# Kernel tuning notes

Measured on AMD Instinct MI355X. Metric: run time of the kernel, lower is better.

## Reference

```python
import jax, jax.numpy as jnp
import numpy as np

N_NODES = 10000
N_EDGES = 80000
IN_DIM = 768
HID = 256
HEADS = 8
NEG_SLOPE = 0.2


def setup_inputs() -> dict:
    key = jax.random.key(0)
    ks = jax.random.split(key, 12)
    s = 0.02
    x = jax.random.normal(ks[0], (N_NODES, IN_DIM), dtype=jnp.float32)
    edge_index = jax.random.randint(ks[1], (2, N_EDGES), 0, N_NODES, dtype=jnp.int64)
    W1 = jax.random.normal(ks[2], (IN_DIM, HEADS * HID), dtype=jnp.float32) * s
    a_src1 = jax.random.normal(ks[3], (HEADS, HID), dtype=jnp.float32) * s
    a_dst1 = jax.random.normal(ks[4], (HEADS, HID), dtype=jnp.float32) * s
    b1 = jnp.zeros((HEADS * HID,), dtype=jnp.float32)
    W2 = jax.random.normal(ks[5], (HEADS * HID, HEADS * HID), dtype=jnp.float32) * s
    a_src2 = jax.random.normal(ks[6], (HEADS, HID), dtype=jnp.float32) * s
    a_dst2 = jax.random.normal(ks[7], (HEADS, HID), dtype=jnp.float32) * s
    b2 = jnp.zeros((HID,), dtype=jnp.float32)
    # graph_projection: 256 -> 256
    Wp = jax.random.normal(ks[8], (HID, HID), dtype=jnp.float32) * s
    bp = jnp.zeros((HID,), dtype=jnp.float32)
    return dict(x=x, edge_index=edge_index, W1=W1, a_src1=a_src1, a_dst1=a_dst1,
                b1=b1, W2=W2, a_src2=a_src2, a_dst2=a_dst2, b2=b2, Wp=Wp, bp=bp)


def _gat_conv(x, src, dst, W, a_src, a_dst, b, concat):
    """PyG GATConv (eval mode, self-loops already appended to src/dst)."""
    N = x.shape[0]
    H, C = a_src.shape
    h = (x @ W).reshape(N, H, C)                         # [N,H,C] per-head projection
    alpha_s = jnp.sum(h * a_src[None], axis=-1)           # [N,H]
    alpha_d = jnp.sum(h * a_dst[None], axis=-1)           # [N,H]
    e = jax.nn.leaky_relu(alpha_s[src] + alpha_d[dst], NEG_SLOPE)  # [E,H]
    # segment softmax over incoming edges of each dst node
    m = jax.ops.segment_max(e, dst, num_segments=N)       # [N,H]
    m = jnp.where(jnp.isfinite(m), m, 0.0)
    p = jnp.exp(e - m[dst])
    denom = jax.ops.segment_sum(p, dst, num_segments=N)   # [N,H]
    alpha = p / (denom[dst] + 1e-16)                      # [E,H]
    out = jax.ops.segment_sum(alpha[:, :, None] * h[src], dst, num_segments=N)  # [N,H,C]
    if concat:
        return out.reshape(N, H * C) + b
    return out.mean(axis=1) + b


def reference(x, edge_index, W1, a_src1, a_dst1, b1, W2, a_src2, a_dst2, b2, Wp, bp):
    N = x.shape[0]
    loops = jnp.arange(N, dtype=edge_index.dtype)
    src = jnp.concatenate([edge_index[0], loops])
    dst = jnp.concatenate([edge_index[1], loops])
    h = _gat_conv(x, src, dst, W1, a_src1, a_dst1, b1, concat=True)   # [N, 2048]
    h = jax.nn.elu(h)                                                 # dropout: eval/no-op
    h = _gat_conv(h, src, dst, W2, a_src2, a_dst2, b2, concat=False)  # [N, 256]
    h = h @ Wp + bp
    return jax.nn.relu(h)                                             # dropout: eval/no-op
```

## Files before the change

### kernel.cpp

```cpp
#include <hip/hip_runtime.h>
#include <cstdint>
#include <cstddef>

#define IN_DIM  768
#define NNODES  10000
#define MPAD    10240
#define NEDGES  80000
#define E_TOT   90000
#define HEADS   8
#define HID     256
#define HC      2048
#define NEG_SLOPE 0.2f

#define CVT_BLK  ((MPAD * IN_DIM / 4) / 256)
#define CNT_BLK  ((E_TOT + 255) / 256)
#define T1_BLK   ((HC / 32) * (IN_DIM / 32))
#define T2_BLK   ((HC / 32) * (HC / 32))
#define TP_BLK   ((HID / 32) * (HID / 32))
#define PREP_BLK (CVT_BLK + CNT_BLK + T1_BLK + T2_BLK + TP_BLK)

typedef _Float16 __attribute__((ext_vector_type(8))) f16x8;
typedef float    __attribute__((ext_vector_type(4))) f32x4;

__device__ __forceinline__ int edge_src(const int* __restrict__ ei, int e) {
    return (e < NEDGES) ? ei[e] : (e - NEDGES);
}
__device__ __forceinline__ int edge_dst(const int* __restrict__ ei, int e) {
    return (e < NEDGES) ? ei[NEDGES + e] : (e - NEDGES);
}

__device__ __forceinline__ void tcvt_body(
    const float* __restrict__ W, _Float16* __restrict__ T,
    int K, int N, int bx, int by, int t)
{
    __shared__ float tile[32][33];
    int tx = t & 31, ty = t >> 5;
#pragma unroll
    for (int q = 0; q < 4; q++)
        tile[ty + q * 8][tx] = W[(size_t)(by * 32 + ty + q * 8) * N + bx * 32 + tx];
    __syncthreads();
#pragma unroll
    for (int q = 0; q < 4; q++) {
        float v = tile[tx][ty + q * 8];
        T[(size_t)(bx * 32 + ty + q * 8) * K + by * 32 + tx] = (_Float16)v;
    }
}

__global__ __launch_bounds__(256) void prep_kernel(
    const float* __restrict__ x, _Float16* __restrict__ xh,
    const int* __restrict__ ei, int* __restrict__ cnt,
    const float* __restrict__ W1, _Float16* __restrict__ W1t,
    const float* __restrict__ W2, _Float16* __restrict__ W2t,
    const float* __restrict__ Wp, _Float16* __restrict__ Wpt)
{
    int b = blockIdx.x;
    int t = threadIdx.x;
    if (b < CVT_BLK) {
        int i = b * 256 + t;
        size_t e = (size_t)i * 4;
        int r = (int)(e / IN_DIM);
        float4 v = (r < NNODES) ? *(const float4*)(x + e)
                                : make_float4(0.f, 0.f, 0.f, 0.f);
        _Float16 h4[4] = {(_Float16)v.x, (_Float16)v.y, (_Float16)v.z, (_Float16)v.w};
        *(ushort4*)(xh + e) = *(ushort4*)h4;
    } else if (b < CVT_BLK + CNT_BLK) {
        int e = (b - CVT_BLK) * 256 + t;
        if (e < E_TOT) atomicAdd(&cnt[edge_dst(ei, e)], 1);
    } else if (b < CVT_BLK + CNT_BLK + T1_BLK) {
        int idx = b - (CVT_BLK + CNT_BLK);
        tcvt_body(W1, W1t, IN_DIM, HC, idx % (HC / 32), idx / (HC / 32), t);
    } else if (b < CVT_BLK + CNT_BLK + T1_BLK + T2_BLK) {
        int idx = b - (CVT_BLK + CNT_BLK + T1_BLK);
        tcvt_body(W2, W2t, HC, HC, idx % (HC / 32), idx / (HC / 32), t);
    } else {
        int idx = b - (CVT_BLK + CNT_BLK + T1_BLK + T2_BLK);
        tcvt_body(Wp, Wpt, HID, HID, idx % (HID / 32), idx / (HID / 32), t);
    }
}

__global__ void scan_kernel(const int* __restrict__ cnt, int* __restrict__ indptr) {
    __shared__ int sums[1024];
    const int CH = 10;
    int t = threadIdx.x;
    int base = t * CH;
    int s = 0;
#pragma unroll
    for (int i = 0; i < CH; i++) { int idx = base + i; if (idx < NNODES) s += cnt[idx]; }
    sums[t] = s;
    __syncthreads();
    for (int off = 1; off < 1024; off <<= 1) {
        int v = (t >= off) ? sums[t - off] : 0;
        __syncthreads();
        sums[t] += v;
        __syncthreads();
    }
    int run = (t == 0) ? 0 : sums[t - 1];
#pragma unroll
    for (int i = 0; i < CH; i++) {
        int idx = base + i;
        if (idx < NNODES) { indptr[idx] = run; run += cnt[idx]; }
    }
    if (t == 0) indptr[NNODES] = E_TOT;
}

__global__ void scatter_kernel(const int* __restrict__ ei, const int* __restrict__ indptr,
                               int* __restrict__ cur, int* __restrict__ sorted) {
    int e = blockIdx.x * 256 + threadIdx.x;
    if (e < E_TOT) {
        int d = edge_dst(ei, e);
        int pos = atomicAdd(&cur[d], 1);
        sorted[indptr[d] + pos] = e;
    }
}

__global__ __launch_bounds__(512, 2) void gemm8p_kernel(
    const _Float16* __restrict__ A, const _Float16* __restrict__ B,
    _Float16* __restrict__ C, int M, int K, int Nn)
{
    __shared__ __align__(16) _Float16 lds[2][36864];

    const int t = threadIdx.x;
    const int w = t >> 6, lane = t & 63;
    const int fr = lane & 15, q4 = lane >> 4;
    const int wr = w >> 2, wc = w & 3;

    const int nwgx = gridDim.x;
    int wg = blockIdx.y * nwgx + blockIdx.x;
    const int cpx = (nwgx * gridDim.y) >> 3;
    wg = (wg & 7) * cpx + (wg >> 3);
    const int row0 = (wg / nwgx) * 320;
    const int col0 = (wg % nwgx) * 256;

    const int rowt = t >> 3;
    const int scol = ((t & 7) ^ (rowt & 7)) << 3;
    const _Float16* baseA = A + (size_t)(row0 + rowt) * K + scol;
    const _Float16* baseB = B + (size_t)(col0 + rowt) * K + scol;
    const int dstw = w * 512;

    auto stageA = [&](int q, int kel, int bb) {
        __builtin_amdgcn_global_load_lds(
            (const __attribute__((address_space(1))) void*)(baseA + (size_t)q * 64 * K + kel),
            (__attribute__((address_space(3))) void*)&lds[bb][q * 4096 + dstw], 16, 0, 0);
    };
    auto stageB = [&](int q, int kel, int bb) {
        __builtin_amdgcn_global_load_lds(
            (const __attribute__((address_space(1))) void*)(baseB + (size_t)q * 64 * K + kel),
            (__attribute__((address_space(3))) void*)&lds[bb][20480 + q * 4096 + dstw], 16, 0, 0);
    };

    f32x4 acc[2][2][5][2];
#pragma unroll
    for (int qm = 0; qm < 2; qm++)
#pragma unroll
        for (int qn = 0; qn < 2; qn++)
#pragma unroll
            for (int mi = 0; mi < 5; mi++)
#pragma unroll
                for (int ni = 0; ni < 2; ni++)
                    acc[qm][qn][mi][ni] = {0.f, 0.f, 0.f, 0.f};

    f16x8 fa[5][2], fb[2][2];

#define LOADA(BB, QM)                                                           \
    {                                                                           \
        _Pragma("unroll")                                                       \
        for (int mi = 0; mi < 5; mi++) {                                        \
            _Pragma("unroll")                                                   \
            for (int ks = 0; ks < 2; ks++) {                                    \
                int lr = wr * 80 + mi * 16 + fr;                                \
                int sl = ((ks << 2) | q4) ^ (fr & 7);                           \
                fa[mi][ks] = *(const f16x8*)&lds[BB][(QM) * 10240 + (lr << 6) + (sl << 3)]; \
            }                                                                   \
        }                                                                       \
    }
#define LOADB(BB, QN)                                                           \
    {                                                                           \
        _Pragma("unroll")                                                       \
        for (int ni = 0; ni < 2; ni++) {                                        \
            _Pragma("unroll")                                                   \
            for (int ks = 0; ks < 2; ks++) {                                    \
                int lr = wc * 32 + ni * 16 + fr;                                \
                int sl = ((ks << 2) | q4) ^ (fr & 7);                           \
                fb[ni][ks] = *(const f16x8*)&lds[BB][20480 + (QN) * 8192 + (lr << 6) + (sl << 3)]; \
            }                                                                   \
        }                                                                       \
    }

#define PHASE(QM, QN, LOAD_STMT, STAGE_STMT, WAIT_STMT)                         \
    do {                                                                        \
        WAIT_STMT;                                                              \
        __builtin_amdgcn_s_barrier();                                           \
        LOAD_STMT;                                                              \
        STAGE_STMT;                                                             \
        asm volatile("s_waitcnt lgkmcnt(0)" ::: "memory");                      \
        __builtin_amdgcn_sched_barrier(0);                                      \
        __builtin_amdgcn_s_setprio(1);                                          \
        _Pragma("unroll")                                                       \
        for (int ks = 0; ks < 2; ks++) {                                        \
            _Pragma("unroll")                                                   \
            for (int mi = 0; mi < 5; mi++) {                                    \
                _Pragma("unroll")                                               \
                for (int ni = 0; ni < 2; ni++)                                  \
                    acc[QM][QN][mi][ni] = __builtin_amdgcn_mfma_f32_16x16x32_f16(\
                        fa[mi][ks], fb[ni][ks], acc[QM][QN][mi][ni], 0, 0, 0);  \
            }                                                                   \
        }                                                                       \
        __builtin_amdgcn_s_setprio(0);                                          \
        __builtin_amdgcn_sched_barrier(0);                                      \
    } while (0)

#define VM(N) asm volatile("s_waitcnt vmcnt(" #N ")" ::: "memory")

    stageA(0, 0, 0); stageA(1, 0, 0); stageA(2, 0, 0);
    stageB(0, 0, 0); stageB(1, 0, 0);
    stageB(2, 0, 0); stageB(3, 0, 0);
    stageA(3, 0, 0); stageA(4, 0, 0);

    const int nT = K >> 6;
    int t0 = 0;
    for (; t0 < nT - 1; ++t0) {
        int bb = t0 & 1;
        int bn = bb ^ 1;
        int k1 = (t0 + 1) << 6;
        PHASE(0, 0, { LOADA(bb, 0); LOADB(bb, 0); },
              { stageA(0, k1, bn); stageA(1, k1, bn); stageA(2, k1, bn); },
              VM(4));
        PHASE(0, 1, { LOADB(bb, 1); },
              { stageB(0, k1, bn); stageB(1, k1, bn); },
              VM(5));
        PHASE(1, 1, { LOADA(bb, 1); },
              { stageB(2, k1, bn); stageB(3, k1, bn); },
              VM(5));
        PHASE(1, 0, { LOADB(bb, 0); },
              { stageA(3, k1, bn); stageA(4, k1, bn); },
              ((void)0));
    }
    {
        int bb = t0 & 1;
        PHASE(0, 0, { LOADA(bb, 0); LOADB(bb, 0); }, ((void)0), VM(4));
        PHASE(0, 1, { LOADB(bb, 1); },               ((void)0), VM(2));
        PHASE(1, 1, { LOADA(bb, 1); },               ((void)0), VM(0));
        PHASE(1, 0, { LOADB(bb, 0); },               ((void)0), ((void)0));
    }
#undef PHASE
#undef LOADA
#undef LOADB
#undef VM

#pragma unroll
    for (int qm = 0; qm < 2; qm++)
#pragma unroll
        for (int qn = 0; qn < 2; qn++)
#pragma unroll
            for (int mi = 0; mi < 5; mi++) {
                int mb = row0 + qm * 160 + wr * 80 + mi * 16 + q4 * 4;
#pragma unroll
                for (int ni = 0; ni < 2; ni++) {
                    int n = col0 + qn * 128 + wc * 32 + ni * 16 + fr;
#pragma unroll
                    for (int r = 0; r < 4; r++) {
                        int m = mb + r;
                        if (m < M) C[(size_t)m * Nn + n] = (_Float16)acc[qm][qn][mi][ni][r];
                    }
                }
            }
}

template <int EPI>
__global__ __launch_bounds__(256) void mfma_gemm_kernel(
    const _Float16* __restrict__ A, const _Float16* __restrict__ B,
    void* __restrict__ Cout, const float* __restrict__ bias,
    int M, int K, int Nn, int swz)
{
    __shared__ __align__(16) _Float16 sA[2][128 * 32];
    __shared__ __align__(16) _Float16 sB[2][128 * 32];

    int t = threadIdx.x;
    int bx = blockIdx.x, by = blockIdx.y;
    if (swz) {
        int id = by * 16 + bx;
        int xcd = id & 7, slot = id >> 3;
        bx = 2 * xcd + (slot & 1);
        by = slot >> 1;
    }
    int row0 = by * 128;
    int col0 = bx * 128;

    int s0 = t, s1 = t + 256;
    int m0 = s0 >> 2, k0 = (s0 & 3) * 8;
    int m1 = s1 >> 2, k1 = (s1 & 3) * 8;
    const _Float16* a0 = A + (size_t)(row0 + m0) * K + k0;
    const _Float16* a1 = A + (size_t)(row0 + m1) * K + k1;
    const _Float16* b0 = B + (size_t)(col0 + m0) * K + k0;
    const _Float16* b1 = B + (size_t)(col0 + m1) * K + k1;

    int w = t >> 6, lane = t & 63;
    int wm = (w & 1) * 64, wn = (w >> 1) * 64;
    int fr = lane & 15, quad = lane >> 4;

    auto stage = [&](int kt, int bsel) {
        _Float16* dA0 = &sA[bsel][(w * 64) * 8];
        _Float16* dA1 = &sA[bsel][(w * 64 + 256) * 8];
        _Float16* dB0 = &sB[bsel][(w * 64) * 8];
        _Float16* dB1 = &sB[bsel][(w * 64 + 256) * 8];
        __builtin_amdgcn_global_load_lds(
            (const __attribute__((address_space(1))) void*)(a0 + kt),
            (__attribute__((address_space(3))) void*)dA0, 16, 0, 0);
        __builtin_amdgcn_global_load_lds(
            (const __attribute__((address_space(1))) void*)(a1 + kt),
            (__attribute__((address_space(3))) void*)dA1, 16, 0, 0);
        __builtin_amdgcn_global_load_lds(
            (const __attribute__((address_space(1))) void*)(b0 + kt),
            (__attribute__((address_space(3))) void*)dB0, 16, 0, 0);
        __builtin_amdgcn_global_load_lds(
            (const __attribute__((address_space(1))) void*)(b1 + kt),
            (__attribute__((address_space(3))) void*)dB1, 16, 0, 0);
    };

    f32x4 acc[4][4];
#pragma unroll
    for (int i = 0; i < 4; i++)
#pragma unroll
        for (int j = 0; j < 4; j++) acc[i][j] = {0.f, 0.f, 0.f, 0.f};

    const int nIt = K / 32;
    stage(0, 0);
    __syncthreads();

    for (int it = 0; it < nIt; ++it) {
        int cb = it & 1;
        if (it + 1 < nIt) stage((it + 1) * 32, cb ^ 1);

        f16x8 fa[4], fb[4];
#pragma unroll
        for (int i = 0; i < 4; i++) {
            fa[i] = *(const f16x8*)&sA[cb][(wm + i * 16 + fr) * 32 + quad * 8];
            fb[i] = *(const f16x8*)&sB[cb][(wn + i * 16 + fr) * 32 + quad * 8];
        }
#pragma unroll
        for (int i = 0; i < 4; i++)
#pragma unroll
            for (int j = 0; j < 4; j++)
                acc[i][j] = __builtin_amdgcn_mfma_f32_16x16x32_f16(fa[i], fb[j], acc[i][j], 0, 0, 0);

        if (it + 1 < nIt) __syncthreads();
    }

    if (EPI == 0) {
        _Float16* C = (_Float16*)Cout;
#pragma unroll
        for (int i = 0; i < 4; i++) {
            int mbase = row0 + wm + i * 16 + quad * 4;
#pragma unroll
            for (int j = 0; j < 4; j++) {
                int n = col0 + wn + j * 16 + fr;
#pragma unroll
                for (int r = 0; r < 4; r++) {
                    int m = mbase + r;
                    if (m < M) C[(size_t)m * Nn + n] = (_Float16)acc[i][j][r];
                }
            }
        }
    } else {
        float* C = (float*)Cout;
        float bv[4];
#pragma unroll
        for (int j = 0; j < 4; j++) bv[j] = bias[col0 + wn + j * 16 + fr];
#pragma unroll
        for (int i = 0; i < 4; i++) {
            int mbase = row0 + wm + i * 16 + quad * 4;
#pragma unroll
            for (int j = 0; j < 4; j++) {
                int n = col0 + wn + j * 16 + fr;
#pragma unroll
                for (int r = 0; r < 4; r++) {
                    int m = mbase + r;
                    if (m < M) C[(size_t)m * Nn + n] = fmaxf(acc[i][j][r] + bv[j], 0.f);
                }
            }
        }
    }
}

__global__ __launch_bounds__(256) void attn_kernel(
    const _Float16* __restrict__ H, const float* __restrict__ a_src,
    const float* __restrict__ a_dst, float* __restrict__ as_out,
    float* __restrict__ ad_out)
{
    int n = blockIdx.x;
    int t = threadIdx.x;
    int h = t >> 5, l = t & 31;
    f16x8 hv = *(const f16x8*)&H[(size_t)n * HC + h * HID + l * 8];
    const float* asp = a_src + h * HID + l * 8;
    const float* adp = a_dst + h * HID + l * 8;
    float sa = 0.f, sd = 0.f;
#pragma unroll
    for (int q = 0; q < 8; q++) {
        float v = (float)hv[q];
        sa = fmaf(v, asp[q], sa);
        sd = fmaf(v, adp[q], sd);
    }
#pragma unroll
    for (int o = 16; o > 0; o >>= 1) {
        sa += __shfl_xor(sa, o, 32);
        sd += __shfl_xor(sd, o, 32);
    }
    if (l == 0) { as_out[n * HEADS + h] = sa; ad_out[n * HEADS + h] = sd; }
}

template <int MODE>
__global__ __launch_bounds__(256) void agg_kernel(
    const _Float16* __restrict__ H, const float* __restrict__ as_,
    const float* __restrict__ ad_, const float* __restrict__ bias,
    const int* __restrict__ indptr, const int* __restrict__ sorted,
    const int* __restrict__ ei, _Float16* __restrict__ outh)
{
    __shared__ float m8[HEADS], d8[HEADS], adl[HEADS];
    __shared__ int   srcl[64];
    __shared__ float al2[HEADS][64];
    __shared__ float red[HC];

    int n = blockIdx.x;
    int t = threadIdx.x;

    if (n >= NNODES) {
        if (MODE == 0) {
            _Float16 z8[8] = {};
            *(f16x8*)&outh[(size_t)n * HC + t * 8] = *(f16x8*)z8;
        } else {
            outh[(size_t)n * HID + t] = (_Float16)0.f;
        }
        return;
    }

    int start = indptr[n];
    int deg = indptr[n + 1] - start;

    if (t < HEADS) adl[t] = ad_[n * HEADS + t];
    __syncthreads();

    int hh = t >> 5, c8 = (t & 31) * 8;
    const size_t hoff = (size_t)hh * HID + c8;
    float acc[8] = {};

    if (deg <= 64) {
        if (t < deg) srcl[t] = edge_src(ei, sorted[start + t]);
        __syncthreads();
        {
            int j = t & 63, h0 = t >> 6;
            if (j < deg) {
                int s = srcl[j];
#pragma unroll
                for (int q = 0; q < 2; q++) {
                    int hx = h0 + q * 4;
                    float v = as_[s * HEADS + hx] + adl[hx];
                    v = (v >= 0.f) ? v : NEG_SLOPE * v;
                    al2[hx][j] = v;
                }
            }
        }
        __syncthreads();
        {
            int h = t >> 5, l = t & 31;
            float mx = -1e30f;
            for (int jj = l; jj < deg; jj += 32) mx = fmaxf(mx, al2[h][jj]);
#pragma unroll
            for (int o = 16; o > 0; o >>= 1) mx = fmaxf(mx, __shfl_xor(mx, o, 32));
            float sm = 0.f;
            for (int jj = l; jj < deg; jj += 32) {
                float e = expf(al2[h][jj] - mx);
                al2[h][jj] = e;
                sm += e;
            }
#pragma unroll
            for (int o = 16; o > 0; o >>= 1) sm += __shfl_xor(sm, o, 32);
            float den = sm + 1e-16f;
            for (int jj = l; jj < deg; jj += 32) al2[h][jj] = al2[h][jj] / den;
        }
        __syncthreads();
        int jj = 0;
        for (; jj + 3 < deg; jj += 4) {
            int sx0 = srcl[jj + 0], sx1 = srcl[jj + 1];
            int sx2 = srcl[jj + 2], sx3 = srcl[jj + 3];
            f16x8 h0v = *(const f16x8*)&H[(size_t)sx0 * HC + hoff];
            f16x8 h1v = *(const f16x8*)&H[(size_t)sx1 * HC + hoff];
            f16x8 h2v = *(const f16x8*)&H[(size_t)sx2 * HC + hoff];
            f16x8 h3v = *(const f16x8*)&H[(size_t)sx3 * HC + hoff];
            float4 a4 = *(const float4*)&al2[hh][jj];
#pragma unroll
            for (int q = 0; q < 8; q++) acc[q] = fmaf(a4.x, (float)h0v[q], acc[q]);
#pragma unroll
            for (int q = 0; q < 8; q++) acc[q] = fmaf(a4.y, (float)h1v[q], acc[q]);
#pragma unroll
            for (int q = 0; q < 8; q++) acc[q] = fmaf(a4.z, (float)h2v[q], acc[q]);
#pragma unroll
            for (int q = 0; q < 8; q++) acc[q] = fmaf(a4.w, (float)h3v[q], acc[q]);
        }
        for (; jj < deg; jj++) {
            int s = srcl[jj];
            f16x8 hv = *(const f16x8*)&H[(size_t)s * HC + hoff];
            float a = al2[hh][jj];
#pragma unroll
            for (int q = 0; q < 8; q++)
                acc[q] = fmaf(a, (float)hv[q], acc[q]);
        }
    } else {
        int h = t >> 5, l = t & 31;
        float adh = adl[h];

        float mx = -1e30f;
        for (int j = l; j < deg; j += 32) {
            int e = sorted[start + j];
            int s = edge_src(ei, e);
            float v = as_[s * HEADS + h] + adh;
            v = (v >= 0.f) ? v : NEG_SLOPE * v;
            mx = fmaxf(mx, v);
        }
#pragma unroll
        for (int o = 16; o > 0; o >>= 1) mx = fmaxf(mx, __shfl_xor(mx, o, 32));

        float sm = 0.f;
        for (int j = l; j < deg; j += 32) {
            int e = sorted[start + j];
            int s = edge_src(ei, e);
            float v = as_[s * HEADS + h] + adh;
            v = (v >= 0.f) ? v : NEG_SLOPE * v;
            sm += expf(v - mx);
        }
#pragma unroll
        for (int o = 16; o > 0; o >>= 1) sm += __shfl_xor(sm, o, 32);
        if (l == 0) { m8[h] = mx; d8[h] = sm; }

        for (int base = 0; base < deg; base += 64) {
            int cntc = min(64, deg - base);
            __syncthreads();
            if (t < cntc) srcl[t] = edge_src(ei, sorted[start + base + t]);
            __syncthreads();
            {
                int j = t & 63, h0 = t >> 6;
                if (j < cntc) {
                    int s = srcl[j];
#pragma unroll
                    for (int q = 0; q < 2; q++) {
                        int hx = h0 + q * 4;
                        float v = as_[s * HEADS + hx] + adl[hx];
                        v = (v >= 0.f) ? v : NEG_SLOPE * v;
                        al2[hx][j] = expf(v - m8[hx]) / (d8[hx] + 1e-16f);
                    }
                }
            }
            __syncthreads();
            int jj = 0;
            for (; jj + 3 < cntc; jj += 4) {
                int sx0 = srcl[jj + 0], sx1 = srcl[jj + 1];
                int sx2 = srcl[jj + 2], sx3 = srcl[jj + 3];
                f16x8 h0v = *(const f16x8*)&H[(size_t)sx0 * HC + hoff];
                f16x8 h1v = *(const f16x8*)&H[(size_t)sx1 * HC + hoff];
                f16x8 h2v = *(const f16x8*)&H[(size_t)sx2 * HC + hoff];
                f16x8 h3v = *(const f16x8*)&H[(size_t)sx3 * HC + hoff];
                float4 a4 = *(const float4*)&al2[hh][jj];
#pragma unroll
                for (int q = 0; q < 8; q++) acc[q] = fmaf(a4.x, (float)h0v[q], acc[q]);
#pragma unroll
                for (int q = 0; q < 8; q++) acc[q] = fmaf(a4.y, (float)h1v[q], acc[q]);
#pragma unroll
                for (int q = 0; q < 8; q++) acc[q] = fmaf(a4.z, (float)h2v[q], acc[q]);
#pragma unroll
                for (int q = 0; q < 8; q++) acc[q] = fmaf(a4.w, (float)h3v[q], acc[q]);
            }
            for (; jj < cntc; jj++) {
                int s = srcl[jj];
                f16x8 hv = *(const f16x8*)&H[(size_t)s * HC + hoff];
                float a = al2[hh][jj];
#pragma unroll
                for (int q = 0; q < 8; q++)
                    acc[q] = fmaf(a, (float)hv[q], acc[q]);
            }
        }
    }

    if (MODE == 0) {
        _Float16 o8[8];
#pragma unroll
        for (int q = 0; q < 8; q++) {
            float v = acc[q] + bias[hoff + q];
            v = (v > 0.f) ? v : expm1f(v);
            o8[q] = (_Float16)v;
        }
        *(f16x8*)&outh[(size_t)n * HC + hoff] = *(f16x8*)o8;
    } else {
#pragma unroll
        for (int q = 0; q < 8; q++) red[hoff + q] = acc[q];
        __syncthreads();
        float s = 0.f;
#pragma unroll
        for (int h2 = 0; h2 < HEADS; h2++) s += red[h2 * HID + t];
        outh[(size_t)n * HID + t] = (_Float16)(s * 0.125f + bias[t]);
    }
}

extern "C" void kernel_launch(void* const* d_in, const int* in_sizes, int n_in,
                              void* d_out, int out_size, void* d_ws, size_t ws_size,
                              hipStream_t stream)
{
    const float* x      = (const float*)d_in[0];
    const int*   ei     = (const int*)  d_in[1];
    const float* W1     = (const float*)d_in[2];
    const float* a_src1 = (const float*)d_in[3];
    const float* a_dst1 = (const float*)d_in[4];
    const float* b1     = (const float*)d_in[5];
    const float* W2     = (const float*)d_in[6];
    const float* a_src2 = (const float*)d_in[7];
    const float* a_dst2 = (const float*)d_in[8];
    const float* b2     = (const float*)d_in[9];
    const float* Wp     = (const float*)d_in[10];
    const float* bp     = (const float*)d_in[11];
    float* out = (float*)d_out;

    char* ws = (char*)d_ws;
    size_t off = 0;
    auto alloc = [&](size_t bytes) -> char* {
        char* p = ws + off;
        off += (bytes + 255) & ~(size_t)255;
        return p;
    };
    _Float16* Hbuf = (_Float16*)alloc((size_t)NNODES * HC * 2);
    _Float16* A2   = (_Float16*)alloc((size_t)MPAD * HC * 2);
    _Float16* W1t  = (_Float16*)alloc((size_t)HC * IN_DIM * 2);
    _Float16* W2t  = (_Float16*)alloc((size_t)HC * HC * 2);
    _Float16* Wpt  = (_Float16*)alloc((size_t)HID * HID * 2);
    _Float16* xh   = (_Float16*)alloc((size_t)MPAD * IN_DIM * 2);
    _Float16* out2h = (_Float16*)alloc((size_t)MPAD * HID * 2);
    float* asad   = (float*)alloc((size_t)4 * NNODES * HEADS * sizeof(float));
    float* as1 = asad;
    float* ad1 = asad + (size_t)NNODES * HEADS;
    float* as2 = asad + (size_t)2 * NNODES * HEADS;
    float* ad2 = asad + (size_t)3 * NNODES * HEADS;
    int*   cntcur = (int*)alloc((size_t)2 * NNODES * sizeof(int));
    int*   cnt = cntcur;
    int*   cur = cntcur + NNODES;
    int*   indptr = (int*)  alloc((size_t)(NNODES + 1) * sizeof(int));
    int*   sorted = (int*)  alloc((size_t)E_TOT * sizeof(int));

    hipMemsetAsync(cntcur, 0, (size_t)2 * NNODES * sizeof(int), stream);
    prep_kernel<<<PREP_BLK, 256, 0, stream>>>(x, xh, ei, cnt,
                                              W1, W1t, W2, W2t, Wp, Wpt);
    scan_kernel<<<1, 1024, 0, stream>>>(cnt, indptr);
    scatter_kernel<<<(E_TOT + 255) / 256, 256, 0, stream>>>(ei, indptr, cur, sorted);

    dim3 g8(HC / 256, MPAD / 320);

    gemm8p_kernel<<<g8, 512, 0, stream>>>(xh, W1t, Hbuf, NNODES, IN_DIM, HC);
    attn_kernel<<<NNODES, 256, 0, stream>>>(Hbuf, a_src1, a_dst1, as1, ad1);
    agg_kernel<0><<<MPAD, 256, 0, stream>>>(Hbuf, as1, ad1, b1, indptr, sorted, ei, A2);

    gemm8p_kernel<<<g8, 512, 0, stream>>>(A2, W2t, Hbuf, NNODES, HC, HC);
    attn_kernel<<<NNODES, 256, 0, stream>>>(Hbuf, a_src2, a_dst2, as2, ad2);
    agg_kernel<1><<<MPAD, 256, 0, stream>>>(Hbuf, as2, ad2, b2, indptr, sorted, ei, out2h);

    dim3 gProj(HID / 128, MPAD / 128);
    mfma_gemm_kernel<1><<<gProj, 256, 0, stream>>>(out2h, Wpt, out, bp,
                                                   NNODES, HID, HID, 0);
}
```

Before: 393.4 us.

## Fuse attention-score dot products into GEMM epilogue and simplify pipeline schedule

The per-head source and destination attention dot products are now computed from the fp32 GEMM accumulators in the epilogue, using shuffle and LDS reductions. This removes the separate attn_kernel launch and its re-read of the fp16 H buffer. The K-loop is also restructured: each tile waits on vmcnt(0), issues three phases instead of four with all B staging in one phase, and keeps both B quarters in registers, dropping the peeled last iteration. The risks are added register pressure, a coarser wait that may expose more memory latency, and fp32-versus-fp16 differences in the attention logits.

```diff
diff --git a/kernel.cpp b/kernel.cpp
--- a/kernel.cpp
+++ b/kernel.cpp
@@ -115,7 +115,9 @@
 
 __global__ __launch_bounds__(512, 2) void gemm8p_kernel(
     const _Float16* __restrict__ A, const _Float16* __restrict__ B,
-    _Float16* __restrict__ C, int M, int K, int Nn)
+    _Float16* __restrict__ C, int M, int K, int Nn,
+    const float* __restrict__ asrc, const float* __restrict__ adst,
+    float* __restrict__ as_out, float* __restrict__ ad_out)
 {
     __shared__ __align__(16) _Float16 lds[2][36864];
 
@@ -159,7 +161,7 @@
                 for (int ni = 0; ni < 2; ni++)
                     acc[qm][qn][mi][ni] = {0.f, 0.f, 0.f, 0.f};
 
-    f16x8 fa[5][2], fb[2][2];
+    f16x8 fa[5][2], fb[2][2][2];
 
 #define LOADA(BB, QM)                                                           \
     {                                                                           \
@@ -181,20 +183,12 @@
             for (int ks = 0; ks < 2; ks++) {                                    \
                 int lr = wc * 32 + ni * 16 + fr;                                \
                 int sl = ((ks << 2) | q4) ^ (fr & 7);                           \
-                fb[ni][ks] = *(const f16x8*)&lds[BB][20480 + (QN) * 8192 + (lr << 6) + (sl << 3)]; \
+                fb[QN][ni][ks] = *(const f16x8*)&lds[BB][20480 + (QN) * 8192 + (lr << 6) + (sl << 3)]; \
             }                                                                   \
         }                                                                       \
     }
-
-#define PHASE(QM, QN, LOAD_STMT, STAGE_STMT, WAIT_STMT)                         \
-    do {                                                                        \
-        WAIT_STMT;                                                              \
-        __builtin_amdgcn_s_barrier();                                           \
-        LOAD_STMT;                                                              \
-        STAGE_STMT;                                                             \
-        asm volatile("s_waitcnt lgkmcnt(0)" ::: "memory");                      \
-        __builtin_amdgcn_sched_barrier(0);                                      \
-        __builtin_amdgcn_s_setprio(1);                                          \
+#define MFMAQ(QM, QN)                                                           \
+    {                                                                           \
         _Pragma("unroll")                                                       \
         for (int ks = 0; ks < 2; ks++) {                                        \
             _Pragma("unroll")                                                   \
@@ -202,50 +196,46 @@
                 _Pragma("unroll")                                               \
                 for (int ni = 0; ni < 2; ni++)                                  \
                     acc[QM][QN][mi][ni] = __builtin_amdgcn_mfma_f32_16x16x32_f16(\
-                        fa[mi][ks], fb[ni][ks], acc[QM][QN][mi][ni], 0, 0, 0);  \
+                        fa[mi][ks], fb[QN][ni][ks], acc[QM][QN][mi][ni], 0, 0, 0); \
             }                                                                   \
         }                                                                       \
-        __builtin_amdgcn_s_setprio(0);                                          \
-        __builtin_amdgcn_sched_barrier(0);                                      \
-    } while (0)
-
-#define VM(N) asm volatile("s_waitcnt vmcnt(" #N ")" ::: "memory")
+    }
+#define LG0 do { asm volatile("s_waitcnt lgkmcnt(0)" ::: "memory");             \
+                 __builtin_amdgcn_sched_barrier(0); } while (0)
 
     stageA(0, 0, 0); stageA(1, 0, 0); stageA(2, 0, 0);
-    stageB(0, 0, 0); stageB(1, 0, 0);
-    stageB(2, 0, 0); stageB(3, 0, 0);
+    stageB(0, 0, 0); stageB(1, 0, 0); stageB(2, 0, 0); stageB(3, 0, 0);
     stageA(3, 0, 0); stageA(4, 0, 0);
 
     const int nT = K >> 6;
-    int t0 = 0;
-    for (; t0 < nT - 1; ++t0) {
-        int bb = t0 & 1;
-        int bn = bb ^ 1;
-        int k1 = (t0 + 1) << 6;
-        PHASE(0, 0, { LOADA(bb, 0); LOADB(bb, 0); },
-              { stageA(0, k1, bn); stageA(1, k1, bn); stageA(2, k1, bn); },
-              VM(4));
-        PHASE(0, 1, { LOADB(bb, 1); },
-              { stageB(0, k1, bn); stageB(1, k1, bn); },
-              VM(5));
-        PHASE(1, 1, { LOADA(bb, 1); },
-              { stageB(2, k1, bn); stageB(3, k1, bn); },
-              VM(5));
-        PHASE(1, 0, { LOADB(bb, 0); },
-              { stageA(3, k1, bn); stageA(4, k1, bn); },
-              ((void)0));
-    }
-    {
-        int bb = t0 & 1;
-        PHASE(0, 0, { LOADA(bb, 0); LOADB(bb, 0); }, ((void)0), VM(4));
-        PHASE(0, 1, { LOADB(bb, 1); },               ((void)0), VM(2));
-        PHASE(1, 1, { LOADA(bb, 1); },               ((void)0), VM(0));
-        PHASE(1, 0, { LOADB(bb, 0); },               ((void)0), ((void)0));
-    }
-#undef PHASE
+    for (int t0 = 0; t0 < nT; ++t0) {
+        const int bb = t0 & 1, bn = bb ^ 1, k1 = (t0 + 1) << 6;
+        const bool pf = (t0 + 1 < nT);
+        asm volatile("s_waitcnt vmcnt(0)" ::: "memory");
+        __builtin_amdgcn_s_barrier();
+
+        LOADA(bb, 0); LOADB(bb, 0);
+        if (pf) { stageA(0, k1, bn); stageA(1, k1, bn); stageA(2, k1, bn); }
+        LG0;
+        __builtin_amdgcn_s_setprio(1); MFMAQ(0, 0); __builtin_amdgcn_s_setprio(0);
+        __builtin_amdgcn_sched_barrier(0);
+
+        LOADB(bb, 1);
+        if (pf) { stageB(0, k1, bn); stageB(1, k1, bn); stageB(2, k1, bn); stageB(3, k1, bn); }
+        LG0;
+        __builtin_amdgcn_s_setprio(1); MFMAQ(0, 1); __builtin_amdgcn_s_setprio(0);
+        __builtin_amdgcn_sched_barrier(0);
+
+        LOADA(bb, 1);
+        if (pf) { stageA(3, k1, bn); stageA(4, k1, bn); }
+        LG0;
+        __builtin_amdgcn_s_setprio(1); MFMAQ(1, 1); MFMAQ(1, 0); __builtin_amdgcn_s_setprio(0);
+        __builtin_amdgcn_sched_barrier(0);
+    }
 #undef LOADA
 #undef LOADB
-#undef VM
+#undef MFMAQ
+#undef LG0
 
 #pragma unroll
     for (int qm = 0; qm < 2; qm++)
@@ -264,6 +254,58 @@
                     }
                 }
             }
+
+    if (as_out) {
+        __syncthreads();
+        float* sAs = (float*)&lds[0][0];
+        float* sAd = sAs + 320 * 4;
+        float asv[2][2], adv[2][2];
+#pragma unroll
+        for (int qn = 0; qn < 2; qn++)
+#pragma unroll
+            for (int ni = 0; ni < 2; ni++) {
+                int n = col0 + qn * 128 + wc * 32 + ni * 16 + fr;
+                asv[qn][ni] = asrc[n];
+                adv[qn][ni] = adst[n];
+            }
+#pragma unroll
+        for (int qm = 0; qm < 2; qm++)
+#pragma unroll
+            for (int mi = 0; mi < 5; mi++)
+#pragma unroll
+                for (int r = 0; r < 4; r++) {
+                    float sa = 0.f, sd = 0.f;
+#pragma unroll
+                    for (int qn = 0; qn < 2; qn++)
+#pragma unroll
+                        for (int ni = 0; ni < 2; ni++) {
+                            float v = acc[qm][qn][mi][ni][r];
+                            sa = fmaf(v, asv[qn][ni], sa);
+                            sd = fmaf(v, adv[qn][ni], sd);
+                        }
+#pragma unroll
+                    for (int o = 1; o < 16; o <<= 1) {
+                        sa += __shfl_xor(sa, o, 16);
+                        sd += __shfl_xor(sd, o, 16);
+                    }
+                    if (fr == 0) {
+                        int rl = qm * 160 + wr * 80 + mi * 16 + q4 * 4 + r;
+                        sAs[rl * 4 + wc] = sa;
+                        sAd[rl * 4 + wc] = sd;
+                    }
+                }
+        __syncthreads();
+        if (t < 320) {
+            float sa = sAs[t * 4] + sAs[t * 4 + 1] + sAs[t * 4 + 2] + sAs[t * 4 + 3];
+            float sd = sAd[t * 4] + sAd[t * 4 + 1] + sAd[t * 4 + 2] + sAd[t * 4 + 3];
+            int m = row0 + t;
+            if (m < M) {
+                int head = col0 >> 8;
+                as_out[m * HEADS + head] = sa;
+                ad_out[m * HEADS + head] = sd;
+            }
+        }
+    }
 }
 
 template <int EPI>
@@ -380,32 +422,6 @@
             }
         }
     }
-}
-
-__global__ __launch_bounds__(256) void attn_kernel(
-    const _Float16* __restrict__ H, const float* __restrict__ a_src,
-    const float* __restrict__ a_dst, float* __restrict__ as_out,
-    float* __restrict__ ad_out)
-{
-    int n = blockIdx.x;
-    int t = threadIdx.x;
-    int h = t >> 5, l = t & 31;
-    f16x8 hv = *(const f16x8*)&H[(size_t)n * HC + h * HID + l * 8];
-    const float* asp = a_src + h * HID + l * 8;
-    const float* adp = a_dst + h * HID + l * 8;
-    float sa = 0.f, sd = 0.f;
-#pragma unroll
-    for (int q = 0; q < 8; q++) {
-        float v = (float)hv[q];
-        sa = fmaf(v, asp[q], sa);
-        sd = fmaf(v, adp[q], sd);
-    }
-#pragma unroll
-    for (int o = 16; o > 0; o >>= 1) {
-        sa += __shfl_xor(sa, o, 32);
-        sd += __shfl_xor(sd, o, 32);
-    }
-    if (l == 0) { as_out[n * HEADS + h] = sa; ad_out[n * HEADS + h] = sd; }
 }
 
 template <int MODE>
@@ -650,12 +666,12 @@
 
     dim3 g8(HC / 256, MPAD / 320);
 
-    gemm8p_kernel<<<g8, 512, 0, stream>>>(xh, W1t, Hbuf, NNODES, IN_DIM, HC);
-    attn_kernel<<<NNODES, 256, 0, stream>>>(Hbuf, a_src1, a_dst1, as1, ad1);
+    gemm8p_kernel<<<g8, 512, 0, stream>>>(xh, W1t, Hbuf, NNODES, IN_DIM, HC,
+                                          a_src1, a_dst1, as1, ad1);
     agg_kernel<0><<<MPAD, 256, 0, stream>>>(Hbuf, as1, ad1, b1, indptr, sorted, ei, A2);
 
-    gemm8p_kernel<<<g8, 512, 0, stream>>>(A2, W2t, Hbuf, NNODES, HC, HC);
-    attn_kernel<<<NNODES, 256, 0, stream>>>(Hbuf, a_src2, a_dst2, as2, ad2);
+    gemm8p_kernel<<<g8, 512, 0, stream>>>(A2, W2t, Hbuf, NNODES, HC, HC,
+                                          a_src2, a_dst2, as2, ad2);
     agg_kernel<1><<<MPAD, 256, 0, stream>>>(Hbuf, as2, ad2, b2, indptr, sorted, ei, out2h);
 
     dim3 gProj(HID / 128, MPAD / 128);
```

Measured after the change: 407.8 us. +3.7%, slower.
